# Performance work log

Hardware: AMD Instinct MI355X
Metric: run time of the kernel (lower is better)

## Reference

```python
import jax, jax.numpy as jnp
import numpy as np

B, N, D, E = 8, 1024, 128, 8


def setup_inputs() -> dict:
    key = jax.random.key(0)
    k1, k2, k3, k4 = jax.random.split(key, 4)
    node_state = jax.random.normal(k1, (B, N, D), dtype=jnp.float32)
    edge_type_mat = jax.random.uniform(k2, (B, N, N, E), dtype=jnp.float32)
    adj_mat = jax.random.randint(k3, (B, N, N), 0, 2).astype(jnp.float32)  # 0/1 valued
    W = jax.random.normal(k4, (E, D, D), dtype=jnp.float32)
    return {"node_state": node_state, "edge_type_mat": edge_type_mat,
            "adj_mat": adj_mat, "W": W}


def reference(node_state, edge_type_mat, adj_mat, W):
    # Faithful to the torch einsum chain:
    #   mp[b,s,o,i,j]  = edge_type[b,s,o,e] W[e,i,j]
    #   sm[b,s,i,j]    = adj[b,s,o] mp[b,s,o,i,j]
    #   out[b,s,i]     = sm[b,s,i,j] node_state[b,s,j]   (note: node_state at s, not o)
    # Reordered to avoid the O(n^2 d^2) intermediate:
    # coef[b,s,e] = sum_o adj[b,s,o] * edge_type[b,s,o,e]
    coef = jnp.einsum('bso,bsoe->bse', adj_mat, edge_type_mat)
    # v[b,s,e,i] = W[e] @ node_state[b,s]
    v = jnp.einsum('eij,bsj->bsei', W, node_state)
    # out[b,s,i] = sum_e coef[b,s,e] * v[b,s,e,i]
    return jnp.einsum('bse,bsei->bsi', coef, v)
```

## Files before the change

kernel.cpp:

```cpp
#include <hip/hip_runtime.h>

constexpr int B_ = 8, N_ = 1024, D_ = 128, E_ = 8;
constexpr int ROWS = B_ * N_;

typedef __attribute__((ext_vector_type(8))) _Float16 f16x8;
typedef __attribute__((ext_vector_type(4))) float f32x4;

__global__ __launch_bounds__(128)
void coef_kernel(const float* __restrict__ edge,
                 const float* __restrict__ adj,
                 float* __restrict__ coef)
{
    __shared__ float s_adj[2][N_];
    const int tid  = threadIdx.x;
    const int wv   = tid >> 6;
    const int lane = tid & 63;
    const int row  = blockIdx.x * 2 + wv;

    {
        const float4* ap = (const float4*)(adj + (size_t)row * N_);
        float4* sp = (float4*)s_adj[wv];
        #pragma unroll
        for (int q = 0; q < 4; ++q) sp[q * 64 + lane] = ap[q * 64 + lane];
    }

    const float4* e4 = (const float4*)(edge + (size_t)row * N_ * E_);
    float ax = 0.f, ay = 0.f, az = 0.f, aw = 0.f;
    #pragma unroll 16
    for (int i = 0; i < 32; ++i) {
        float4 ev = e4[i * 64 + lane];
        float a = s_adj[wv][(i * 64 + lane) >> 1];
        ax += a * ev.x; ay += a * ev.y; az += a * ev.z; aw += a * ev.w;
    }
    #pragma unroll
    for (int m = 2; m <= 32; m <<= 1) {
        ax += __shfl_xor(ax, m, 64);
        ay += __shfl_xor(ay, m, 64);
        az += __shfl_xor(az, m, 64);
        aw += __shfl_xor(aw, m, 64);
    }
    if (lane < 2) {
        float4 r; r.x = ax; r.y = ay; r.z = az; r.w = aw;
        ((float4*)(coef + (size_t)row * E_))[lane] = r;
    }
}

__global__ __launch_bounds__(512)
void gemm_kernel(const float* __restrict__ node,
                 const float* __restrict__ coef,
                 const float* __restrict__ W,
                 float* __restrict__ out)
{
    __shared__ _Float16 sW[E_ * 16 * D_];
    const int tid  = threadIdx.x;
    const int cblk = blockIdx.x & 7;
    const int rblk = blockIdx.x >> 3;
    const int cbase = cblk * 16;

    {
        const int lin = tid * 32;
        const int e   = lin >> 11;
        const int rem = lin & 2047;
        const int i16 = rem >> 7;
        const int j   = rem & 127;
        const float* gp = W + ((size_t)e * D_ + (cbase + i16)) * D_ + j;
        char* lp = (char*)sW;
        const int xr = (i16 & 7) << 4;
        #pragma unroll
        for (int q = 0; q < 4; ++q) {
            float4 a = ((const float4*)gp)[q * 2];
            float4 b = ((const float4*)gp)[q * 2 + 1];
            f16x8 v;
            v[0] = (_Float16)a.x; v[1] = (_Float16)a.y;
            v[2] = (_Float16)a.z; v[3] = (_Float16)a.w;
            v[4] = (_Float16)b.x; v[5] = (_Float16)b.y;
            v[6] = (_Float16)b.z; v[7] = (_Float16)b.w;
            *(f16x8*)(lp + ((lin * 2 + q * 16) ^ xr)) = v;
        }
    }

    const int wv   = tid >> 6;
    const int lane = tid & 63;
    const int l16  = lane & 15;
    const int lk   = lane >> 4;
    const int rbase = rblk * 128 + wv * 16;
    const int r = rbase + l16;

    float cf[E_];
    {
        const float4* cp = (const float4*)(coef + (size_t)r * E_);
        float4 c0 = cp[0], c1 = cp[1];
        cf[0] = c0.x; cf[1] = c0.y; cf[2] = c0.z; cf[3] = c0.w;
        cf[4] = c1.x; cf[5] = c1.y; cf[6] = c1.z; cf[7] = c1.w;
    }
    const float* xrow = node + (size_t)r * D_;
    float xv[4][8];
    #pragma unroll
    for (int q = 0; q < 4; ++q) {
        const float4* p = (const float4*)(xrow + q * 32 + lk * 8);
        float4 a = p[0], b = p[1];
        xv[q][0] = a.x; xv[q][1] = a.y; xv[q][2] = a.z; xv[q][3] = a.w;
        xv[q][4] = b.x; xv[q][5] = b.y; xv[q][6] = b.z; xv[q][7] = b.w;
    }

    __syncthreads();

    f32x4 acc = {};
    const int xr = (l16 & 7) << 4;
    #pragma unroll
    for (int e = 0; e < E_; ++e) {
        const float cfe = cf[e];
        #pragma unroll
        for (int js = 0; js < 4; ++js) {
            f16x8 af;
            #pragma unroll
            for (int t = 0; t < 8; ++t) af[t] = (_Float16)(cfe * xv[js][t]);
            const int boff = (((e * 16 + l16) * D_ + js * 32 + lk * 8) * 2) ^ xr;
            f16x8 bf = *(const f16x8*)((const char*)sW + boff);
            acc = __builtin_amdgcn_mfma_f32_16x16x32_f16(af, bf, acc, 0, 0, 0);
        }
    }
    const int col = cbase + l16;
    #pragma unroll
    for (int t = 0; t < 4; ++t) {
        out[(size_t)(rbase + lk * 4 + t) * D_ + col] = acc[t];
    }
}

extern "C" void kernel_launch(void* const* d_in, const int* in_sizes, int n_in,
                              void* d_out, int out_size, void* d_ws, size_t ws_size,
                              hipStream_t stream) {
    (void)in_sizes; (void)n_in; (void)out_size; (void)ws_size;
    const float* node = (const float*)d_in[0];
    const float* edge = (const float*)d_in[1];
    const float* adj  = (const float*)d_in[2];
    const float* W    = (const float*)d_in[3];

    float* coefp = (float*)d_ws;

    coef_kernel<<<ROWS / 2, 128, 0, stream>>>(edge, adj, coefp);
    gemm_kernel<<<(ROWS / 128) * 8, 512, 0, stream>>>(node, coefp, W, (float*)d_out);
}
```

Measured before the change: 63.97 us.

## Fuse coefficient reduction and GEMM into one kernel with streamed W slices

Merges the coef reduction and the MFMA GEMM into a single kernel. Each 512-thread block computes the coefficients for 32 rows into shared memory, then computes all 128 output columns, loading one W[e] slice at a time into LDS. This removes the second launch and the round trip of coef through global memory. In exchange, every block now reloads and converts all of W (8x128x128) with two barriers per e-step and no overlap. Grid size drops to 256 blocks, and the loops with unroll 1 may expose memory latency in the edge-streaming phase.

```diff
diff --git a/kernel.cpp b/kernel.cpp
--- a/kernel.cpp
+++ b/kernel.cpp
@@ -6,66 +6,59 @@
 typedef __attribute__((ext_vector_type(8))) _Float16 f16x8;
 typedef __attribute__((ext_vector_type(4))) float f32x4;
 
-__global__ __launch_bounds__(128)
-void coef_kernel(const float* __restrict__ edge,
-                 const float* __restrict__ adj,
-                 float* __restrict__ coef)
+__global__ __launch_bounds__(512)
+void fused_kernel(const float* __restrict__ node,
+                  const float* __restrict__ edge,
+                  const float* __restrict__ adj,
+                  const float* __restrict__ W,
+                  float* __restrict__ out)
 {
-    __shared__ float s_adj[2][N_];
+    __shared__ _Float16 sW[D_ * D_];
+    __shared__ float s_coef[32][E_];
+
     const int tid  = threadIdx.x;
     const int wv   = tid >> 6;
     const int lane = tid & 63;
-    const int row  = blockIdx.x * 2 + wv;
+    const int rbase = blockIdx.x * 32;
 
-    {
-        const float4* ap = (const float4*)(adj + (size_t)row * N_);
-        float4* sp = (float4*)s_adj[wv];
+    #pragma unroll 1
+    for (int r = 0; r < 4; ++r) {
+        const int row = rbase + wv * 4 + r;
+        const float4* e4 = (const float4*)(edge + (size_t)row * (N_ * E_));
+        const float*  ar = adj + (size_t)row * N_;
+        float ax = 0.f, ay = 0.f, az = 0.f, aw = 0.f;
+        #pragma unroll 8
+        for (int i = 0; i < 32; ++i) {
+            float4 ev = e4[i * 64 + lane];
+            float a   = ar[i * 32 + (lane >> 1)];
+            ax += a * ev.x; ay += a * ev.y; az += a * ev.z; aw += a * ev.w;
+        }
         #pragma unroll
-        for (int q = 0; q < 4; ++q) sp[q * 64 + lane] = ap[q * 64 + lane];
+        for (int m = 2; m <= 32; m <<= 1) {
+            ax += __shfl_xor(ax, m, 64);
+            ay += __shfl_xor(ay, m, 64);
+            az += __shfl_xor(az, m, 64);
+            aw += __shfl_xor(aw, m, 64);
+        }
+        if (lane < 2) {
+            float4 v; v.x = ax; v.y = ay; v.z = az; v.w = aw;
+            *(float4*)&s_coef[wv * 4 + r][lane * 4] = v;
+        }
     }
 
-    const float4* e4 = (const float4*)(edge + (size_t)row * N_ * E_);
-    float ax = 0.f, ay = 0.f, az = 0.f, aw = 0.f;
-    #pragma unroll 16
-    for (int i = 0; i < 32; ++i) {
-        float4 ev = e4[i * 64 + lane];
-        float a = s_adj[wv][(i * 64 + lane) >> 1];
-        ax += a * ev.x; ay += a * ev.y; az += a * ev.z; aw += a * ev.w;
-    }
-    #pragma unroll
-    for (int m = 2; m <= 32; m <<= 1) {
-        ax += __shfl_xor(ax, m, 64);
-        ay += __shfl_xor(ay, m, 64);
-        az += __shfl_xor(az, m, 64);
-        aw += __shfl_xor(aw, m, 64);
-    }
-    if (lane < 2) {
-        float4 r; r.x = ax; r.y = ay; r.z = az; r.w = aw;
-        ((float4*)(coef + (size_t)row * E_))[lane] = r;
-    }
-}
+    const int l16 = lane & 15;
+    const int lk  = lane >> 4;
+    const int rt  = wv >> 2;
+    const int ct0 = wv & 3;
+    const int myrow = rbase + rt * 16 + l16;
 
-__global__ __launch_bounds__(512)
-void gemm_kernel(const float* __restrict__ node,
-                 const float* __restrict__ coef,
-                 const float* __restrict__ W,
-                 float* __restrict__ out)
-{
-    __shared__ _Float16 sW[E_ * 16 * D_];
-    const int tid  = threadIdx.x;
-    const int cblk = blockIdx.x & 7;
-    const int rblk = blockIdx.x >> 3;
-    const int cbase = cblk * 16;
-
+    const int si = tid >> 2;
+    const int sj = (tid & 3) * 32;
+    const int sxr = (si & 7) << 4;
+    char* lp = (char*)sW;
+    const int sbyte = (si * D_ + sj) * 2;
     {
-        const int lin = tid * 32;
-        const int e   = lin >> 11;
-        const int rem = lin & 2047;
-        const int i16 = rem >> 7;
-        const int j   = rem & 127;
-        const float* gp = W + ((size_t)e * D_ + (cbase + i16)) * D_ + j;
-        char* lp = (char*)sW;
-        const int xr = (i16 & 7) << 4;
+        const float* gp = W + (size_t)si * D_ + sj;
         #pragma unroll
         for (int q = 0; q < 4; ++q) {
             float4 a = ((const float4*)gp)[q * 2];
@@ -75,25 +68,19 @@
             v[2] = (_Float16)a.z; v[3] = (_Float16)a.w;
             v[4] = (_Float16)b.x; v[5] = (_Float16)b.y;
             v[6] = (_Float16)b.z; v[7] = (_Float16)b.w;
-            *(f16x8*)(lp + ((lin * 2 + q * 16) ^ xr)) = v;
+            *(f16x8*)(lp + ((sbyte + q * 16) ^ sxr)) = v;
         }
     }
-
-    const int wv   = tid >> 6;
-    const int lane = tid & 63;
-    const int l16  = lane & 15;
-    const int lk   = lane >> 4;
-    const int rbase = rblk * 128 + wv * 16;
-    const int r = rbase + l16;
+    __syncthreads();
 
     float cf[E_];
     {
-        const float4* cp = (const float4*)(coef + (size_t)r * E_);
-        float4 c0 = cp[0], c1 = cp[1];
+        float4 c0 = *(const float4*)&s_coef[rt * 16 + l16][0];
+        float4 c1 = *(const float4*)&s_coef[rt * 16 + l16][4];
         cf[0] = c0.x; cf[1] = c0.y; cf[2] = c0.z; cf[3] = c0.w;
         cf[4] = c1.x; cf[5] = c1.y; cf[6] = c1.z; cf[7] = c1.w;
     }
-    const float* xrow = node + (size_t)r * D_;
+    const float* xrow = node + (size_t)myrow * D_;
     float xv[4][8];
     #pragma unroll
     for (int q = 0; q < 4; ++q) {
@@ -103,11 +90,8 @@
         xv[q][4] = b.x; xv[q][5] = b.y; xv[q][6] = b.z; xv[q][7] = b.w;
     }
 
-    __syncthreads();
-
-    f32x4 acc = {};
-    const int xr = (l16 & 7) << 4;
-    #pragma unroll
+    f32x4 acc0 = {}, acc1 = {};
+    #pragma unroll 1
     for (int e = 0; e < E_; ++e) {
         const float cfe = cf[e];
         #pragma unroll
@@ -115,29 +99,49 @@
             f16x8 af;
             #pragma unroll
             for (int t = 0; t < 8; ++t) af[t] = (_Float16)(cfe * xv[js][t]);
-            const int boff = (((e * 16 + l16) * D_ + js * 32 + lk * 8) * 2) ^ xr;
-            f16x8 bf = *(const f16x8*)((const char*)sW + boff);
-            acc = __builtin_amdgcn_mfma_f32_16x16x32_f16(af, bf, acc, 0, 0, 0);
+            const int j = js * 32 + lk * 8;
+            const int b0 = (((ct0 * 16 + l16) * D_ + j) * 2) ^ ((l16 & 7) << 4);
+            const int b1 = ((((ct0 + 4) * 16 + l16) * D_ + j) * 2) ^ ((l16 & 7) << 4);
+            f16x8 bf0 = *(const f16x8*)((const char*)sW + b0);
+            f16x8 bf1 = *(const f16x8*)((const char*)sW + b1);
+            acc0 = __builtin_amdgcn_mfma_f32_16x16x32_f16(af, bf0, acc0, 0, 0, 0);
+            acc1 = __builtin_amdgcn_mfma_f32_16x16x32_f16(af, bf1, acc1, 0, 0, 0);
+        }
+        if (e < E_ - 1) {
+            __syncthreads();
+            const float* gp = W + ((size_t)(e + 1) * D_ + si) * D_ + sj;
+            #pragma unroll
+            for (int q = 0; q < 4; ++q) {
+                float4 a = ((const float4*)gp)[q * 2];
+                float4 b = ((const float4*)gp)[q * 2 + 1];
+                f16x8 v;
+                v[0] = (_Float16)a.x; v[1] = (_Float16)a.y;
+                v[2] = (_Float16)a.z; v[3] = (_Float16)a.w;
+                v[4] = (_Float16)b.x; v[5] = (_Float16)b.y;
+                v[6] = (_Float16)b.z; v[7] = (_Float16)b.w;
+                *(f16x8*)(lp + ((sbyte + q * 16) ^ sxr)) = v;
+            }
+            __syncthreads();
         }
     }
-    const int col = cbase + l16;
+
+    const int col0 = ct0 * 16 + l16;
     #pragma unroll
     for (int t = 0; t < 4; ++t) {
-        out[(size_t)(rbase + lk * 4 + t) * D_ + col] = acc[t];
+        const size_t orow = (size_t)(rbase + rt * 16 + lk * 4 + t) * D_;
+        out[orow + col0]      = acc0[t];
+        out[orow + col0 + 64] = acc1[t];
     }
 }
 
 extern "C" void kernel_launch(void* const* d_in, const int* in_sizes, int n_in,
                               void* d_out, int out_size, void* d_ws, size_t ws_size,
                               hipStream_t stream) {
-    (void)in_sizes; (void)n_in; (void)out_size; (void)ws_size;
+    (void)in_sizes; (void)n_in; (void)out_size; (void)d_ws; (void)ws_size;
     const float* node = (const float*)d_in[0];
     const float* edge = (const float*)d_in[1];
     const float* adj  = (const float*)d_in[2];
     const float* W    = (const float*)d_in[3];
 
-    float* coefp = (float*)d_ws;
-
-    coef_kernel<<<ROWS / 2, 128, 0, stream>>>(edge, adj, coefp);
-    gemm_kernel<<<(ROWS / 128) * 8, 512, 0, stream>>>(node, coefp, W, (float*)d_out);
+    fused_kernel<<<ROWS / 32, 512, 0, stream>>>(node, edge, adj, W, (float*)d_out);
 }
```

Result: slower. 73.04 us (+14.2%).
